# Performance work log

Hardware: AMD Instinct MI355X
Metric: run time of the kernel (lower is better)

## Reference

```python
import math
import jax, jax.numpy as jnp
import numpy as np

B, H, S, D = 2, 16, 2048, 64


def setup_inputs() -> dict:
    key = jax.random.key(0)
    kq, kk, kv = jax.random.split(key, 3)
    Q = jax.random.normal(kq, (B, H, S, D), dtype=jnp.float32)
    K = jax.random.normal(kk, (B, H, S, D), dtype=jnp.float32)
    V = jax.random.normal(kv, (B, H, S, D), dtype=jnp.float32)
    # padding mask: (N, H, query_len), True = keep (module expands with [..., None])
    padding_mask = jnp.ones((B, H, S), dtype=bool)
    # boolean causal attention mask, broadcastable to (B, H, S, S)
    attention_mask = jnp.tril(jnp.ones((S, S), dtype=bool))[None, None]
    return {"Q": Q, "K": K, "V": V,
            "padding_mask": padding_mask, "attention_mask": attention_mask}


def reference(Q, K, V, padding_mask, attention_mask):
    # scores: (B, H, S_q, S_k)
    scale = 1.0 / math.sqrt(K.shape[-1])
    attn = jnp.einsum("bhqd,bhkd->bhqk", Q, K) * scale
    # query-side padding mask (is_query_mask=True): expand last axis
    attn = jnp.where(padding_mask[..., None], attn, -jnp.inf)
    # boolean attention mask
    attn = jnp.where(attention_mask, attn, -jnp.inf)
    attn = jax.nn.softmax(attn, axis=-1)
    # nan-clean: rows fully masked to -inf softmax to NaN -> 0
    attn = jnp.where(jnp.isnan(attn), 0.0, attn)
    return jnp.einsum("bhqk,bhkd->bhqd", attn, V)
```

## Files before the change

### kernel.cpp

```cpp
#include <hip/hip_runtime.h>


typedef __attribute__((ext_vector_type(8))) short bf16x8;
typedef __attribute__((ext_vector_type(4))) float f32x4;
typedef __attribute__((ext_vector_type(4))) short s16x4;
typedef __attribute__((ext_vector_type(2))) unsigned uint2v;

#define MFMA16(a, b, c) __builtin_amdgcn_mfma_f32_16x16x32_bf16(a, b, c, 0, 0, 0)

#define S_LEN 2048
#define D_DIM 64
#define NBH 32

static __device__ __forceinline__ short f2bf(float f) {
  unsigned u = __builtin_bit_cast(unsigned, f);
  u += 0x7fffu + ((u >> 16) & 1u);
  return (short)(u >> 16);
}

static __device__ __forceinline__ unsigned pk2(float a, float b) {
#if __has_builtin(__builtin_amdgcn_cvt_pk_bf16_f32)
  auto r = __builtin_amdgcn_cvt_pk_bf16_f32(a, b);
  return __builtin_bit_cast(unsigned, r);
#else
  return (unsigned)(unsigned short)f2bf(a) |
         ((unsigned)(unsigned short)f2bf(b) << 16);
#endif
}

static __device__ __forceinline__ float fexp2(float x) {
#if __has_builtin(__builtin_amdgcn_exp2f)
  return __builtin_amdgcn_exp2f(x);
#else
  return exp2f(x);
#endif
}

static __device__ __forceinline__ bf16x8 cvt8(const float* p) {
  f32x4 a = *(const f32x4*)p;
  f32x4 b = *(const f32x4*)(p + 4);
  bf16x8 r;
#pragma unroll
  for (int j = 0; j < 4; ++j) { r[j] = f2bf(a[j]); r[j + 4] = f2bf(b[j]); }
  return r;
}

static __device__ __forceinline__ void load_lds16(const short* g, short* l) {
  __builtin_amdgcn_global_load_lds(
      (const __attribute__((address_space(1))) unsigned*)g,
      (__attribute__((address_space(3))) unsigned*)l, 16, 0, 0);
}

__global__ __launch_bounds__(256) void stage(const float* __restrict__ K,
                                             const float* __restrict__ V,
                                             short* __restrict__ Kb,
                                             short* __restrict__ Vt) {
  const int tid = threadIdx.x;
  if (blockIdx.x < 1024) {
    const size_t b0 = (size_t)blockIdx.x * 4096;
#pragma unroll
    for (int p = 0; p < 2; ++p) {
      const size_t i = b0 + p * 2048 + tid * 8;
      f32x4 a = *(const f32x4*)(K + i);
      f32x4 b = *(const f32x4*)(K + i + 4);
      bf16x8 r;
#pragma unroll
      for (int j = 0; j < 4; ++j) { r[j] = f2bf(a[j]); r[j + 4] = f2bf(b[j]); }
      *(bf16x8*)(Kb + i) = r;
    }
  } else {
    __shared__ unsigned t[64][18];
    const int bi = blockIdx.x - 1024;
    const int bh = bi >> 6, k32 = bi & 63;
    const float* src = V + ((size_t)bh * S_LEN + k32 * 32) * D_DIM;
    const int pr = tid & 15;
    const int dq = tid >> 4;
    f32x4 a = *(const f32x4*)(src + (2 * pr)     * D_DIM + dq * 4);
    f32x4 b = *(const f32x4*)(src + (2 * pr + 1) * D_DIM + dq * 4);
#pragma unroll
    for (int j = 0; j < 4; ++j) t[dq * 4 + j][pr] = pk2(a[j], b[j]);
    __syncthreads();
    const int d = tid >> 2, seg = tid & 3;
    uint2v lo = *(const uint2v*)(&t[d][seg * 4]);
    uint2v hi = *(const uint2v*)(&t[d][seg * 4 + 2]);
    short* dst = Vt + (size_t)bh * D_DIM * S_LEN + (size_t)d * S_LEN +
                 k32 * 32 + seg * 8;
    *(uint2v*)(dst)     = lo;
    *(uint2v*)(dst + 4) = hi;
  }
}

__global__ __launch_bounds__(256, 4) void attn_fwd(
    const float* __restrict__ Q, const short* __restrict__ Kb,
    const short* __restrict__ Vt, float* __restrict__ O) {
  __shared__ __align__(16) short kbuf[2][4096];
  __shared__ __align__(16) short vbuf[2][4096];
  __shared__ __align__(16) short pbuf[4][1024];

  const int tid  = threadIdx.x;
  const int wave = tid >> 6;
  const int lane = tid & 63;
  const int quad = lane >> 4;
  const int col  = lane & 15;

  const int bh = blockIdx.x & 31;
  const int i2 = blockIdx.x >> 5;
  const int jj = i2 & 7, gg = i2 >> 3;
  const int qb = (gg & 1) ? (jj + ((gg & 2) << 2))
                          : (31 - jj - ((gg & 2) << 2));
  const int n  = qb + 1;
  const int q0 = qb * 64 + wave * 16;

  const float* Qh = Q  + (size_t)bh * S_LEN * D_DIM;
  const short* Kh = Kb + (size_t)bh * S_LEN * D_DIM;
  const short* Vh = Vt + (size_t)bh * D_DIM * S_LEN;

  const bf16x8 bq0 = cvt8(Qh + (q0 + col) * D_DIM + quad * 8);
  const bf16x8 bq1 = cvt8(Qh + (q0 + col) * D_DIM + quad * 8 + 32);

  const int L0 = tid,       r0s = L0 >> 3, c0s = (L0 & 7) ^ (r0s & 7);
  const int L1 = 256 + tid, r1s = L1 >> 3, c1s = (L1 & 7) ^ (r1s & 7);
  const int wb0 = (wave * 64) * 8;
  const int wb1 = (256 + wave * 64) * 8;

  f32x4 o[4];
#pragma unroll
  for (int i = 0; i < 4; ++i) o[i] = 0.f;
  float psum = 0.f;
  const float sc = 0.125f * 1.44269504088896340736f;

  const int rbase = col * 64;
  const int sw0 = ((quad       ^ (col & 7)) << 3);
  const int sw1 = (((4 + quad) ^ (col & 7)) << 3);
  short* pw = &pbuf[wave][col * 64];
  const int cw0 = (quad >> 1), ho = (quad & 1) << 2;

  auto prefetch = [&](int t, int buf) {
    const int k0n = t << 6;
    load_lds16(Kh + (size_t)(k0n + r0s) * 64 + c0s * 8, &kbuf[buf][wb0]);
    load_lds16(Kh + (size_t)(k0n + r1s) * 64 + c1s * 8, &kbuf[buf][wb1]);
    load_lds16(Vh + (size_t)r0s * S_LEN + k0n + c0s * 8, &vbuf[buf][wb0]);
    load_lds16(Vh + (size_t)r1s * S_LEN + k0n + c1s * 8, &vbuf[buf][wb1]);
  };

  auto body = [&](int t, bool masked) {
    const short* kb = kbuf[t & 1];
    const short* vb = vbuf[t & 1];

    bf16x8 av0[4], av1[4];
#pragma unroll
    for (int mt = 0; mt < 4; ++mt) {
      av0[mt] = *(const bf16x8*)(vb + mt * 1024 + rbase + sw0);
      av1[mt] = *(const bf16x8*)(vb + mt * 1024 + rbase + sw1);
    }

    f32x4 s[4];
#pragma unroll
    for (int mt = 0; mt < 4; ++mt) {
      bf16x8 a0 = *(const bf16x8*)(kb + mt * 1024 + rbase + sw0);
      bf16x8 a1 = *(const bf16x8*)(kb + mt * 1024 + rbase + sw1);
      f32x4 c = 0.f;
      c = MFMA16(a0, bq0, c);
      c = MFMA16(a1, bq1, c);
      s[mt] = c;
    }

    const int k0 = t << 6, qA = q0 + col;
#pragma unroll
    for (int mt = 0; mt < 4; ++mt) {
      float p0 = fexp2(fmaf(s[mt][0], sc, -8.0f));
      float p1 = fexp2(fmaf(s[mt][1], sc, -8.0f));
      float p2 = fexp2(fmaf(s[mt][2], sc, -8.0f));
      float p3 = fexp2(fmaf(s[mt][3], sc, -8.0f));
      if (masked) {
        const int kk = k0 + mt * 16 + quad * 4;
        if (kk     > qA) p0 = 0.f;
        if (kk + 1 > qA) p1 = 0.f;
        if (kk + 2 > qA) p2 = 0.f;
        if (kk + 3 > qA) p3 = 0.f;
      }
      psum += (p0 + p1) + (p2 + p3);
      uint2v u; u[0] = pk2(p0, p1); u[1] = pk2(p2, p3);
      *(uint2v*)(pw + (((2 * mt + cw0) ^ (col & 7)) << 3) + ho) = u;
    }

#pragma unroll
    for (int h = 0; h < 2; ++h) {
      const bf16x8 bp = *(const bf16x8*)(pw + (((h * 4 + quad) ^ (col & 7)) << 3));
#pragma unroll
      for (int mt = 0; mt < 4; ++mt)
        o[mt] = MFMA16(h ? av1[mt] : av0[mt], bp, o[mt]);
    }
  };

  prefetch(0, 0);
  for (int t = 0; t < n - 1; ++t) {
    __syncthreads();
    prefetch(t + 1, (t + 1) & 1);
    body(t, false);
  }
  __syncthreads();
  body(n - 1, true);

  psum += __shfl_xor(psum, 16);
  psum += __shfl_xor(psum, 32);
  const float rl = 1.f / psum;
  float* op = O + (size_t)bh * S_LEN * D_DIM + (size_t)(q0 + col) * D_DIM;
#pragma unroll
  for (int mt = 0; mt < 4; ++mt) {
    f32x4 ov;
#pragma unroll
    for (int r = 0; r < 4; ++r) ov[r] = o[mt][r] * rl;
    *(f32x4*)(op + mt * 16 + quad * 4) = ov;
  }
}

extern "C" void kernel_launch(void* const* d_in, const int* in_sizes, int n_in,
                              void* d_out, int out_size, void* d_ws, size_t ws_size,
                              hipStream_t stream) {
  const float* Q = (const float*)d_in[0];
  const float* K = (const float*)d_in[1];
  const float* V = (const float*)d_in[2];
  short* Kb = (short*)d_ws;
  short* Vt = Kb + (size_t)NBH * S_LEN * D_DIM;
  stage   <<<dim3(3072), dim3(256), 0, stream>>>(K, V, Kb, Vt);
  attn_fwd<<<dim3(1024), dim3(256), 0, stream>>>(Q, Kb, Vt, (float*)d_out);
}
```

Measured before the change: 144.6 us.

## Keep softmax probabilities in registers and permute V staging to match MFMA layout

The probability tile no longer round-trips through LDS. The packed bf16 P values in each lane are bit-cast straight into MFMA B operands. To make the key ordering line up with that register layout, the staging kernel now writes V^T with a permuted key order inside each 32-key block. K fragments are also loaded up front next to the V fragments, and the per-SM occupancy hint is raised from 4 to 5 blocks. This removes LDS stores, loads and bank traffic for P and frees its shared memory, at the cost of more live registers, which the tighter launch bound may push into spills.

```diff
diff --git a/kernel.cpp b/kernel.cpp
--- a/kernel.cpp
+++ b/kernel.cpp
@@ -3,8 +3,8 @@
 
 typedef __attribute__((ext_vector_type(8))) short bf16x8;
 typedef __attribute__((ext_vector_type(4))) float f32x4;
-typedef __attribute__((ext_vector_type(4))) short s16x4;
 typedef __attribute__((ext_vector_type(2))) unsigned uint2v;
+typedef __attribute__((ext_vector_type(4))) unsigned uint4v;
 
 #define MFMA16(a, b, c) __builtin_amdgcn_mfma_f32_16x16x32_bf16(a, b, c, 0, 0, 0)
 
@@ -80,22 +80,21 @@
 #pragma unroll
     for (int j = 0; j < 4; ++j) t[dq * 4 + j][pr] = pk2(a[j], b[j]);
     __syncthreads();
-    const int d = tid >> 2, seg = tid & 3;
-    uint2v lo = *(const uint2v*)(&t[d][seg * 4]);
-    uint2v hi = *(const uint2v*)(&t[d][seg * 4 + 2]);
+    const int d = tid >> 2, g = tid & 3;
+    uint2v lo = *(const uint2v*)(&t[d][2 * g]);
+    uint2v hi = *(const uint2v*)(&t[d][8 + 2 * g]);
     short* dst = Vt + (size_t)bh * D_DIM * S_LEN + (size_t)d * S_LEN +
-                 k32 * 32 + seg * 8;
+                 k32 * 32 + g * 8;
     *(uint2v*)(dst)     = lo;
     *(uint2v*)(dst + 4) = hi;
   }
 }
 
-__global__ __launch_bounds__(256, 4) void attn_fwd(
+__global__ __launch_bounds__(256, 5) void attn_fwd(
     const float* __restrict__ Q, const short* __restrict__ Kb,
     const short* __restrict__ Vt, float* __restrict__ O) {
   __shared__ __align__(16) short kbuf[2][4096];
   __shared__ __align__(16) short vbuf[2][4096];
-  __shared__ __align__(16) short pbuf[4][1024];
 
   const int tid  = threadIdx.x;
   const int wave = tid >> 6;
@@ -132,8 +131,6 @@
   const int rbase = col * 64;
   const int sw0 = ((quad       ^ (col & 7)) << 3);
   const int sw1 = (((4 + quad) ^ (col & 7)) << 3);
-  short* pw = &pbuf[wave][col * 64];
-  const int cw0 = (quad >> 1), ho = (quad & 1) << 2;
 
   auto prefetch = [&](int t, int buf) {
     const int k0n = t << 6;
@@ -147,7 +144,12 @@
     const short* kb = kbuf[t & 1];
     const short* vb = vbuf[t & 1];
 
-    bf16x8 av0[4], av1[4];
+    bf16x8 ak0[4], ak1[4], av0[4], av1[4];
+#pragma unroll
+    for (int mt = 0; mt < 4; ++mt) {
+      ak0[mt] = *(const bf16x8*)(kb + mt * 1024 + rbase + sw0);
+      ak1[mt] = *(const bf16x8*)(kb + mt * 1024 + rbase + sw1);
+    }
 #pragma unroll
     for (int mt = 0; mt < 4; ++mt) {
       av0[mt] = *(const bf16x8*)(vb + mt * 1024 + rbase + sw0);
@@ -157,14 +159,13 @@
     f32x4 s[4];
 #pragma unroll
     for (int mt = 0; mt < 4; ++mt) {
-      bf16x8 a0 = *(const bf16x8*)(kb + mt * 1024 + rbase + sw0);
-      bf16x8 a1 = *(const bf16x8*)(kb + mt * 1024 + rbase + sw1);
       f32x4 c = 0.f;
-      c = MFMA16(a0, bq0, c);
-      c = MFMA16(a1, bq1, c);
+      c = MFMA16(ak0[mt], bq0, c);
+      c = MFMA16(ak1[mt], bq1, c);
       s[mt] = c;
     }
 
+    unsigned u[8];
     const int k0 = t << 6, qA = q0 + col;
 #pragma unroll
     for (int mt = 0; mt < 4; ++mt) {
@@ -180,17 +181,20 @@
         if (kk + 3 > qA) p3 = 0.f;
       }
       psum += (p0 + p1) + (p2 + p3);
-      uint2v u; u[0] = pk2(p0, p1); u[1] = pk2(p2, p3);
-      *(uint2v*)(pw + (((2 * mt + cw0) ^ (col & 7)) << 3) + ho) = u;
-    }
-
-#pragma unroll
-    for (int h = 0; h < 2; ++h) {
-      const bf16x8 bp = *(const bf16x8*)(pw + (((h * 4 + quad) ^ (col & 7)) << 3));
-#pragma unroll
-      for (int mt = 0; mt < 4; ++mt)
-        o[mt] = MFMA16(h ? av1[mt] : av0[mt], bp, o[mt]);
-    }
+      u[2 * mt]     = pk2(p0, p1);
+      u[2 * mt + 1] = pk2(p2, p3);
+    }
+
+    uint4v dv0, dv1;
+    dv0[0] = u[0]; dv0[1] = u[1]; dv0[2] = u[2]; dv0[3] = u[3];
+    dv1[0] = u[4]; dv1[1] = u[5]; dv1[2] = u[6]; dv1[3] = u[7];
+    const bf16x8 bp0 = __builtin_bit_cast(bf16x8, dv0);
+    const bf16x8 bp1 = __builtin_bit_cast(bf16x8, dv1);
+
+#pragma unroll
+    for (int mt = 0; mt < 4; ++mt) o[mt] = MFMA16(av0[mt], bp0, o[mt]);
+#pragma unroll
+    for (int mt = 0; mt < 4; ++mt) o[mt] = MFMA16(av1[mt], bp1, o[mt]);
   };
 
   prefetch(0, 0);
```

Result: no change. 142.0 us (-1.8%).
